# Performance work log

Measured on AMD Instinct MI355X. Metric: run time of the kernel, lower is better.

Reference implementation:

```python
import jax, jax.numpy as jnp
import numpy as np

N_NODES = 50000
N_EDGES = 800000
D = 64
L = 2


def setup_inputs() -> dict:
    key = jax.random.key(0)
    ks = jax.random.split(key, 5)
    h = jax.random.normal(ks[0], (N_NODES, D), dtype=jnp.float32)
    Ws = jax.random.normal(ks[1], (L, D, D), dtype=jnp.float32) / np.sqrt(D)
    bs = jnp.zeros((L, D), dtype=jnp.float32)
    edge_weight = jax.random.uniform(ks[2], (N_EDGES,), dtype=jnp.float32)
    src = jax.random.randint(ks[3], (N_EDGES,), 0, N_NODES, dtype=jnp.int64)
    dst = jax.random.randint(ks[4], (N_EDGES,), 0, N_NODES, dtype=jnp.int64)
    return {"h": h, "Ws": Ws, "bs": bs, "edge_weight": edge_weight, "src": src, "dst": dst}


def reference(h, Ws, bs, edge_weight, src, dst):
    # DGL GraphConv(norm='none', activation=relu) with in_feats==out_feats:
    # aggregate-then-transform: agg[v] = sum_{e:(u->v)} w_e * h[u]; h' = relu(agg @ W + b)
    n = h.shape[0]
    for l in range(Ws.shape[0]):
        msg = h[src] * edge_weight[:, None]                      # [E, D] gather + scale
        agg = jax.ops.segment_sum(msg, dst, num_segments=n)      # [N, D] scatter-add
        h = jax.nn.relu(agg @ Ws[l] + bs[l])
    return h
```

## Files before the change

kernel.cpp:

```cpp
#include <hip/hip_runtime.h>
#include <hip/hip_fp16.h>

#define NN 50000
#define NE 800000
#define DD 64
#define BS 64
#define NB 782
#define ECAP 1280
#define CHUNK 3200
#define NPB 250
#define NITEMS (NN * DD / 8)

typedef __attribute__((ext_vector_type(8))) short short8;
typedef __attribute__((ext_vector_type(4))) float f32x4;

__device__ __forceinline__ unsigned packh2(float lo, float hi) {
    __half2 h = __floats2half2_rn(lo, hi);
    return *reinterpret_cast<unsigned*>(&h);
}

__global__ __launch_bounds__(256) void f32_to_f16_zero_kernel(
        const float4* __restrict__ in4, uint4* __restrict__ out4,
        int* __restrict__ gpos, const float* __restrict__ Ws,
        uint4* __restrict__ wfrag) {
    if (blockIdx.x == 0) {
        for (int j = threadIdx.x; j < NB; j += 256) gpos[j] = 0;
    }
    if (blockIdx.x == 1 || blockIdx.x == 2) {
        int L = blockIdx.x - 1;
        const float* W = Ws + L * DD * DD;
        for (int e = threadIdx.x; e < 512; e += 256) {
            int w = e >> 7, s = (e >> 6) & 1, l = e & 63;
            int col = w * 16 + (l & 15);
            int k0 = 32 * s + 8 * (l >> 4);
            uint4 u;
            unsigned* up = (unsigned*)&u;
            #pragma unroll
            for (int uu = 0; uu < 4; ++uu)
                up[uu] = packh2(W[(k0 + 2 * uu) * DD + col],
                                W[(k0 + 2 * uu + 1) * DD + col]);
            wfrag[L * 512 + e] = u;
        }
    }
    int i = blockIdx.x * blockDim.x + threadIdx.x;
    if (i >= NITEMS) return;
    float4 a = in4[2 * i], b = in4[2 * i + 1];
    uint4 o;
    o.x = packh2(a.x, a.y); o.y = packh2(a.z, a.w);
    o.z = packh2(b.x, b.y); o.w = packh2(b.z, b.w);
    out4[i] = o;
}

__global__ __launch_bounds__(1024) void partition_kernel(
        const int* __restrict__ src, const int* __restrict__ dst,
        const float* __restrict__ ew,
        int* __restrict__ gpos, uint2* __restrict__ ebuf) {
    __shared__ int hist[NB];
    __shared__ int base[NB];
    int t = threadIdx.x;
    int c0 = blockIdx.x * CHUNK;
    for (int j = t; j < NB; j += 1024) hist[j] = 0;
    __syncthreads();
    short rank[4];
    int dcache[4];
    #pragma unroll
    for (int i = 0; i < 4; ++i) {
        int o = i * 1024 + t;
        if (o < CHUNK) {
            int d = dst[c0 + o];
            dcache[i] = d;
            rank[i] = (short)atomicAdd(&hist[d >> 6], 1);
        }
    }
    __syncthreads();
    for (int j = t; j < NB; j += 1024) {
        int c = hist[j];
        base[j] = c ? atomicAdd(&gpos[j], c) : 0;
    }
    __syncthreads();
    #pragma unroll
    for (int i = 0; i < 4; ++i) {
        int o = i * 1024 + t;
        if (o < CHUNK) {
            int e = c0 + o;
            int d = dcache[i];
            int bkt = d >> 6;
            int dl = d & 63;
            int pos = base[bkt] + (int)rank[i];
            if (pos < ECAP) {
                ebuf[(size_t)bkt * ECAP + pos] =
                    make_uint2((unsigned)src[e] | ((unsigned)dl << 16),
                               __float_as_uint(ew[e]));
            }
        }
    }
}

__global__ __launch_bounds__(512) void sort_layer0_kernel(
        const uint2* __restrict__ ebuf, const int* __restrict__ gpos,
        const uint2* __restrict__ hh,
        const uint4* __restrict__ wfrag,
        const float* __restrict__ bvec,
        unsigned* __restrict__ sorted, int4* __restrict__ nodespan,
        void* __restrict__ h1out) {
    __shared__ unsigned led[ECAP];
    __shared__ int hist[BS], sc[BS];
    __shared__ int dh[128], dsc[128];
    __shared__ int4 nsp[BS];
    __shared__ unsigned Ahf[BS * 36];
    __shared__ float Dls[BS * 68];
    int t = threadIdx.x;
    int b = blockIdx.x;
    int cnt = min(gpos[b], ECAP);
    const uint2* slab = ebuf + (size_t)b * ECAP;

    if (t < BS) hist[t] = 0;
    if (t < 128) dh[t] = 0;
    __syncthreads();

    unsigned pay[3];
    int dl[3], rk[3];
    #pragma unroll
    for (int i = 0; i < 3; ++i) {
        int o = i * 512 + t;
        if (o < cnt) {
            uint2 q = slab[o];
            dl[i] = (int)(q.x >> 16);
            unsigned w16 = (unsigned)__half_as_ushort(
                __float2half(__uint_as_float(q.y)));
            pay[i] = (q.x & 0xFFFFu) | (w16 << 16);
            rk[i] = atomicAdd(&hist[dl[i]], 1);
        }
    }
    __syncthreads();
    if (t < BS) sc[t] = hist[t];
    __syncthreads();
    #pragma unroll
    for (int off = 1; off < BS; off <<= 1) {
        int v = (t < BS && t >= off) ? sc[t - off] : 0;
        __syncthreads();
        if (t < BS) sc[t] += v;
        __syncthreads();
    }
    unsigned* oslab = sorted + (size_t)b * ECAP;
    #pragma unroll
    for (int i = 0; i < 3; ++i) {
        int o = i * 512 + t;
        if (o < cnt) {
            int pos = sc[dl[i]] - hist[dl[i]] + rk[i];
            led[pos] = pay[i];
            oslab[pos] = pay[i];
        }
    }
    int nn_b = min(BS, NN - b * BS);
    if (t < nn_b) atomicAdd(&dh[min(hist[t], 127)], 1);
    __syncthreads();
    if (t < 128) dsc[t] = dh[t];
    __syncthreads();
    #pragma unroll
    for (int off = 1; off < 128; off <<= 1) {
        int v = (t < 128 && t >= off) ? dsc[t - off] : 0;
        __syncthreads();
        if (t < 128) dsc[t] += v;
        __syncthreads();
    }
    if (t < 128) dh[t] = dsc[t] - dh[t];
    __syncthreads();
    if (t < nn_b) {
        int d = min(hist[t], 127);
        int p = atomicAdd(&dh[d], 1);
        nsp[p] = make_int4(sc[t] - hist[t], hist[t], b * BS + t, 0);
        nodespan[b * BS + p] =
            make_int4(b * ECAP + sc[t] - hist[t], hist[t], b * BS + t, 0);
    } else if (t < BS) {
        nsp[t] = make_int4(0, 0, NN, 0);
        nodespan[b * BS + t] = make_int4(b * ECAP, 0, NN, 0);
    }
    __syncthreads();

    int lane = t & 15;
    unsigned ul = (unsigned)lane;
    __half2 z = __floats2half2_rn(0.f, 0.f);
    #pragma unroll
    for (int pass = 0; pass < 2; ++pass) {
        int g = (t >> 4) + pass * 32;
        int4 sp = nsp[g];
        const unsigned* lrow = led + sp.x;
        int deg = sp.y;
        __half2 a0 = z, a1 = z, b0 = z, b1 = z, c0 = z, c1 = z, d0 = z, d1 = z;
        int j = 0;
        for (; j + 4 <= deg; j += 4) {
            unsigned q0 = lrow[j + 0], q1 = lrow[j + 1];
            unsigned q2 = lrow[j + 2], q3 = lrow[j + 3];
            uint2 r0 = hh[(q0 & 0xFFFFu) * 16u + ul];
            uint2 r1 = hh[(q1 & 0xFFFFu) * 16u + ul];
            uint2 r2 = hh[(q2 & 0xFFFFu) * 16u + ul];
            uint2 r3 = hh[(q3 & 0xFFFFu) * 16u + ul];
            __half2 w0 = __half2half2(__ushort_as_half((unsigned short)(q0 >> 16)));
            __half2 w1 = __half2half2(__ushort_as_half((unsigned short)(q1 >> 16)));
            __half2 w2 = __half2half2(__ushort_as_half((unsigned short)(q2 >> 16)));
            __half2 w3 = __half2half2(__ushort_as_half((unsigned short)(q3 >> 16)));
            a0 = __hfma2(w0, *(const __half2*)&r0.x, a0);
            a1 = __hfma2(w0, *(const __half2*)&r0.y, a1);
            b0 = __hfma2(w1, *(const __half2*)&r1.x, b0);
            b1 = __hfma2(w1, *(const __half2*)&r1.y, b1);
            c0 = __hfma2(w2, *(const __half2*)&r2.x, c0);
            c1 = __hfma2(w2, *(const __half2*)&r2.y, c1);
            d0 = __hfma2(w3, *(const __half2*)&r3.x, d0);
            d1 = __hfma2(w3, *(const __half2*)&r3.y, d1);
        }
        for (; j < deg; ++j) {
            unsigned q0 = lrow[j];
            uint2 r0 = hh[(q0 & 0xFFFFu) * 16u + ul];
            __half2 w0 = __half2half2(__ushort_as_half((unsigned short)(q0 >> 16)));
            a0 = __hfma2(w0, *(const __half2*)&r0.x, a0);
            a1 = __hfma2(w0, *(const __half2*)&r0.y, a1);
        }
        a0 = __hadd2(__hadd2(a0, b0), __hadd2(c0, d0));
        a1 = __hadd2(__hadd2(a1, b1), __hadd2(c1, d1));
        Ahf[g * 36 + 2 * lane]     = *reinterpret_cast<unsigned*>(&a0);
        Ahf[g * 36 + 2 * lane + 1] = *reinterpret_cast<unsigned*>(&a1);
    }
    __syncthreads();

    {
        int w = t >> 6;
        int l = t & 63;
        #pragma unroll
        for (int i = 0; i < 2; ++i) {
            int T = w + 8 * i;
            int rt = T >> 2, ct = T & 3;
            const uint4* arow = (const uint4*)&Ahf[(rt * 16 + (l & 15)) * 36];
            uint4 au0 = arow[l >> 4];
            uint4 au1 = arow[4 + (l >> 4)];
            uint4 bu0 = wfrag[(ct * 2 + 0) * 64 + l];
            uint4 bu1 = wfrag[(ct * 2 + 1) * 64 + l];
            f32x4 d = {0.f, 0.f, 0.f, 0.f};
            d = __builtin_amdgcn_mfma_f32_16x16x32_f16(
                    *(const short8*)&au0, *(const short8*)&bu0, d, 0, 0, 0);
            d = __builtin_amdgcn_mfma_f32_16x16x32_f16(
                    *(const short8*)&au1, *(const short8*)&bu1, d, 0, 0, 0);
            #pragma unroll
            for (int r = 0; r < 4; ++r)
                Dls[(rt * 16 + (l >> 4) * 4 + r) * 68 + ct * 16 + (l & 15)] = d[r];
        }
    }
    __syncthreads();

    #pragma unroll
    for (int i = 0; i < 2; ++i) {
        int idx = i * 512 + t;
        int g2 = idx >> 4, ln = idx & 15;
        float4 bias = reinterpret_cast<const float4*>(bvec)[ln];
        float4 dv = *reinterpret_cast<const float4*>(&Dls[g2 * 68 + ln * 4]);
        float4 o;
        o.x = fmaxf(dv.x + bias.x, 0.f);
        o.y = fmaxf(dv.y + bias.y, 0.f);
        o.z = fmaxf(dv.z + bias.z, 0.f);
        o.w = fmaxf(dv.w + bias.w, 0.f);
        int node = nsp[g2].z;
        if (node < NN) {
            reinterpret_cast<uint2*>(h1out)[(size_t)node * 16 + ln] =
                make_uint2(packh2(o.x, o.y), packh2(o.z, o.w));
        }
    }
}

__global__ __launch_bounds__(512) void gcn_layer1_kernel(
        const uint2* __restrict__ hh,
        const unsigned* __restrict__ sorted,
        const int* __restrict__ gpos,
        const int4* __restrict__ nodespan,
        const uint4* __restrict__ wfrag,
        const float* __restrict__ bvec,
        float4* __restrict__ outp) {
    __shared__ unsigned led[ECAP];
    __shared__ int4 nsp[BS];
    __shared__ unsigned Ahf[BS * 36];
    __shared__ float Dls[BS * 68];
    int t = threadIdx.x;
    int b = blockIdx.x;
    int cnt = min(gpos[b], ECAP);
    const unsigned* slab = sorted + (size_t)b * ECAP;

    #pragma unroll
    for (int i = 0; i < 3; ++i) {
        int o = i * 512 + t;
        if (o < cnt) led[o] = slab[o];
    }
    if (t < BS) {
        int4 sp = nodespan[b * BS + t];
        sp.x -= b * ECAP;
        nsp[t] = sp;
    }
    __syncthreads();

    int lane = t & 15;
    unsigned ul = (unsigned)lane;
    __half2 z = __floats2half2_rn(0.f, 0.f);
    #pragma unroll
    for (int pass = 0; pass < 2; ++pass) {
        int g = (t >> 4) + pass * 32;
        int4 sp = nsp[g];
        const unsigned* lrow = led + sp.x;
        int deg = sp.y;
        __half2 a0 = z, a1 = z, b0 = z, b1 = z, c0 = z, c1 = z, d0 = z, d1 = z;
        int j = 0;
        for (; j + 4 <= deg; j += 4) {
            unsigned q0 = lrow[j + 0], q1 = lrow[j + 1];
            unsigned q2 = lrow[j + 2], q3 = lrow[j + 3];
            uint2 r0 = hh[(q0 & 0xFFFFu) * 16u + ul];
            uint2 r1 = hh[(q1 & 0xFFFFu) * 16u + ul];
            uint2 r2 = hh[(q2 & 0xFFFFu) * 16u + ul];
            uint2 r3 = hh[(q3 & 0xFFFFu) * 16u + ul];
            __half2 w0 = __half2half2(__ushort_as_half((unsigned short)(q0 >> 16)));
            __half2 w1 = __half2half2(__ushort_as_half((unsigned short)(q1 >> 16)));
            __half2 w2 = __half2half2(__ushort_as_half((unsigned short)(q2 >> 16)));
            __half2 w3 = __half2half2(__ushort_as_half((unsigned short)(q3 >> 16)));
            a0 = __hfma2(w0, *(const __half2*)&r0.x, a0);
            a1 = __hfma2(w0, *(const __half2*)&r0.y, a1);
            b0 = __hfma2(w1, *(const __half2*)&r1.x, b0);
            b1 = __hfma2(w1, *(const __half2*)&r1.y, b1);
            c0 = __hfma2(w2, *(const __half2*)&r2.x, c0);
            c1 = __hfma2(w2, *(const __half2*)&r2.y, c1);
            d0 = __hfma2(w3, *(const __half2*)&r3.x, d0);
            d1 = __hfma2(w3, *(const __half2*)&r3.y, d1);
        }
        for (; j < deg; ++j) {
            unsigned q0 = lrow[j];
            uint2 r0 = hh[(q0 & 0xFFFFu) * 16u + ul];
            __half2 w0 = __half2half2(__ushort_as_half((unsigned short)(q0 >> 16)));
            a0 = __hfma2(w0, *(const __half2*)&r0.x, a0);
            a1 = __hfma2(w0, *(const __half2*)&r0.y, a1);
        }
        a0 = __hadd2(__hadd2(a0, b0), __hadd2(c0, d0));
        a1 = __hadd2(__hadd2(a1, b1), __hadd2(c1, d1));
        Ahf[g * 36 + 2 * lane]     = *reinterpret_cast<unsigned*>(&a0);
        Ahf[g * 36 + 2 * lane + 1] = *reinterpret_cast<unsigned*>(&a1);
    }
    __syncthreads();

    {
        int w = t >> 6;
        int l = t & 63;
        #pragma unroll
        for (int i = 0; i < 2; ++i) {
            int T = w + 8 * i;
            int rt = T >> 2, ct = T & 3;
            const uint4* arow = (const uint4*)&Ahf[(rt * 16 + (l & 15)) * 36];
            uint4 au0 = arow[l >> 4];
            uint4 au1 = arow[4 + (l >> 4)];
            uint4 bu0 = wfrag[(ct * 2 + 0) * 64 + l];
            uint4 bu1 = wfrag[(ct * 2 + 1) * 64 + l];
            f32x4 d = {0.f, 0.f, 0.f, 0.f};
            d = __builtin_amdgcn_mfma_f32_16x16x32_f16(
                    *(const short8*)&au0, *(const short8*)&bu0, d, 0, 0, 0);
            d = __builtin_amdgcn_mfma_f32_16x16x32_f16(
                    *(const short8*)&au1, *(const short8*)&bu1, d, 0, 0, 0);
            #pragma unroll
            for (int r = 0; r < 4; ++r)
                Dls[(rt * 16 + (l >> 4) * 4 + r) * 68 + ct * 16 + (l & 15)] = d[r];
        }
    }
    __syncthreads();

    #pragma unroll
    for (int i = 0; i < 2; ++i) {
        int idx = i * 512 + t;
        int g2 = idx >> 4, ln = idx & 15;
        float4 bias = reinterpret_cast<const float4*>(bvec)[ln];
        float4 dv = *reinterpret_cast<const float4*>(&Dls[g2 * 68 + ln * 4]);
        float4 o;
        o.x = fmaxf(dv.x + bias.x, 0.f);
        o.y = fmaxf(dv.y + bias.y, 0.f);
        o.z = fmaxf(dv.z + bias.z, 0.f);
        o.w = fmaxf(dv.w + bias.w, 0.f);
        int node = nsp[g2].z;
        if (node < NN) outp[(size_t)node * 16 + ln] = o;
    }
}

extern "C" void kernel_launch(void* const* d_in, const int* in_sizes, int n_in,
                              void* d_out, int out_size, void* d_ws, size_t ws_size,
                              hipStream_t stream) {
    const float4* h4  = (const float4*)d_in[0];
    const float*  Ws  = (const float*)d_in[1];
    const float*  bsv = (const float*)d_in[2];
    const float*  ew  = (const float*)d_in[3];
    const int*    src = (const int*)d_in[4];
    const int*    dst = (const int*)d_in[5];
    float4* out = (float4*)d_out;
    char* ws = (char*)d_ws;

    int*      gpos     = (int*)(ws);
    uint2*    ebuf     = (uint2*)(ws + 64 * 1024);
    unsigned* sorted   = (unsigned*)(ws + 9u * 1024 * 1024);
    uint4*    wfrag    = (uint4*)(ws + 13u * 1024 * 1024);
    int4*     nodespan = (int4*)(ws + 13u * 1024 * 1024 + 256 * 1024);
    uint2*    h_hf     = (uint2*)(ws + 14u * 1024 * 1024 + 512 * 1024);
    void*     h1       = (void*)(ws + 24u * 1024 * 1024);

    f32_to_f16_zero_kernel<<<(NITEMS + 255) / 256, 256, 0, stream>>>(
        h4, (uint4*)h_hf, gpos, Ws, wfrag);
    partition_kernel<<<NPB, 1024, 0, stream>>>(src, dst, ew, gpos, ebuf);
    sort_layer0_kernel<<<NB, 512, 0, stream>>>(
        ebuf, gpos, h_hf, wfrag, bsv, sorted, nodespan, h1);
    gcn_layer1_kernel<<<NB, 512, 0, stream>>>(
        (const uint2*)h1, sorted, gpos, nodespan, wfrag + 512, bsv + DD, out);
}
```

Baseline: 59.99 us.

## Replace global-atomic edge partition with per-chunk sub-slabs and fuse conversion kernel

The f16 conversion and weight-fragment prep are merged into the partition launch as extra blocks. Partitioning now drops the global atomic counter array: each chunk writes its per-bucket counts to a 2D count table and its edges into fixed-size per-(bucket, chunk) sub-slabs. The sort kernel prefix-sums the 250 chunk counts and gathers the sub-slabs into shared memory, and it records the per-bucket total for layer 1. This removes one launch, the zeroing step and the global atomics. In exchange, the sort kernel does a strided gather of many small slabs with serial per-thread loops, and edges beyond SUBCAP per chunk-bucket pair are silently dropped.

```diff
diff --git a/kernel.cpp b/kernel.cpp
--- a/kernel.cpp
+++ b/kernel.cpp
@@ -7,8 +7,10 @@
 #define BS 64
 #define NB 782
 #define ECAP 1280
+#define SUBCAP 24
 #define CHUNK 3200
 #define NPB 250
+#define KCONV 141
 #define NITEMS (NN * DD / 8)
 
 typedef __attribute__((ext_vector_type(8))) short short8;
@@ -19,103 +21,122 @@
     return *reinterpret_cast<unsigned*>(&h);
 }
 
-__global__ __launch_bounds__(256) void f32_to_f16_zero_kernel(
-        const float4* __restrict__ in4, uint4* __restrict__ out4,
-        int* __restrict__ gpos, const float* __restrict__ Ws,
-        uint4* __restrict__ wfrag) {
-    if (blockIdx.x == 0) {
-        for (int j = threadIdx.x; j < NB; j += 256) gpos[j] = 0;
-    }
-    if (blockIdx.x == 1 || blockIdx.x == 2) {
-        int L = blockIdx.x - 1;
-        const float* W = Ws + L * DD * DD;
-        for (int e = threadIdx.x; e < 512; e += 256) {
-            int w = e >> 7, s = (e >> 6) & 1, l = e & 63;
-            int col = w * 16 + (l & 15);
-            int k0 = 32 * s + 8 * (l >> 4);
-            uint4 u;
-            unsigned* up = (unsigned*)&u;
-            #pragma unroll
-            for (int uu = 0; uu < 4; ++uu)
-                up[uu] = packh2(W[(k0 + 2 * uu) * DD + col],
-                                W[(k0 + 2 * uu + 1) * DD + col]);
-            wfrag[L * 512 + e] = u;
-        }
-    }
-    int i = blockIdx.x * blockDim.x + threadIdx.x;
-    if (i >= NITEMS) return;
-    float4 a = in4[2 * i], b = in4[2 * i + 1];
-    uint4 o;
-    o.x = packh2(a.x, a.y); o.y = packh2(a.z, a.w);
-    o.z = packh2(b.x, b.y); o.w = packh2(b.z, b.w);
-    out4[i] = o;
-}
-
-__global__ __launch_bounds__(1024) void partition_kernel(
+__global__ __launch_bounds__(1024) void build_kernel(
+        const float4* __restrict__ in4,
+        uint4* __restrict__ out4,
+        const float* __restrict__ Ws,
+        uint4* __restrict__ wfrag,
         const int* __restrict__ src, const int* __restrict__ dst,
         const float* __restrict__ ew,
-        int* __restrict__ gpos, uint2* __restrict__ ebuf) {
-    __shared__ int hist[NB];
-    __shared__ int base[NB];
+        int* __restrict__ cnt2d,
+        uint2* __restrict__ ebuf2) {
+    int bid = blockIdx.x;
     int t = threadIdx.x;
-    int c0 = blockIdx.x * CHUNK;
-    for (int j = t; j < NB; j += 1024) hist[j] = 0;
-    __syncthreads();
-    short rank[4];
-    int dcache[4];
-    #pragma unroll
-    for (int i = 0; i < 4; ++i) {
-        int o = i * 1024 + t;
-        if (o < CHUNK) {
-            int d = dst[c0 + o];
-            dcache[i] = d;
-            rank[i] = (short)atomicAdd(&hist[d >> 6], 1);
-        }
-    }
-    __syncthreads();
-    for (int j = t; j < NB; j += 1024) {
-        int c = hist[j];
-        base[j] = c ? atomicAdd(&gpos[j], c) : 0;
-    }
-    __syncthreads();
-    #pragma unroll
-    for (int i = 0; i < 4; ++i) {
-        int o = i * 1024 + t;
-        if (o < CHUNK) {
-            int e = c0 + o;
-            int d = dcache[i];
-            int bkt = d >> 6;
-            int dl = d & 63;
-            int pos = base[bkt] + (int)rank[i];
-            if (pos < ECAP) {
-                ebuf[(size_t)bkt * ECAP + pos] =
-                    make_uint2((unsigned)src[e] | ((unsigned)dl << 16),
-                               __float_as_uint(ew[e]));
+
+    if (bid < NPB) {
+        __shared__ int hist[NB];
+        int c0 = bid * CHUNK;
+        for (int j = t; j < NB; j += 1024) hist[j] = 0;
+        __syncthreads();
+        short rank[4];
+        int dcache[4];
+        #pragma unroll
+        for (int i = 0; i < 4; ++i) {
+            int o = i * 1024 + t;
+            if (o < CHUNK) {
+                int d = dst[c0 + o];
+                dcache[i] = d;
+                rank[i] = (short)atomicAdd(&hist[d >> 6], 1);
             }
         }
+        __syncthreads();
+        for (int j = t; j < NB; j += 1024) cnt2d[(size_t)bid * NB + j] = hist[j];
+        #pragma unroll
+        for (int i = 0; i < 4; ++i) {
+            int o = i * 1024 + t;
+            if (o < CHUNK) {
+                int e = c0 + o;
+                int d = dcache[i];
+                int bkt = d >> 6;
+                int dl = d & 63;
+                int pos = (int)rank[i];
+                if (pos < SUBCAP) {
+                    ebuf2[((size_t)bkt * NPB + bid) * SUBCAP + pos] =
+                        make_uint2((unsigned)src[e] | ((unsigned)dl << 16),
+                                   __float_as_uint(ew[e]));
+                }
+            }
+        }
+    } else {
+        int vb = bid - NPB;
+        if (vb == 0) {
+            int L = t >> 9;
+            int ei = t & 511;
+            if (L < 2) {
+                int w = ei >> 7, s = (ei >> 6) & 1, l = ei & 63;
+                const float* W = Ws + L * DD * DD;
+                int col = w * 16 + (l & 15);
+                int k0 = 32 * s + 8 * (l >> 4);
+                uint4 u;
+                unsigned* up = (unsigned*)&u;
+                #pragma unroll
+                for (int uu = 0; uu < 4; ++uu)
+                    up[uu] = packh2(W[(k0 + 2 * uu) * DD + col],
+                                    W[(k0 + 2 * uu + 1) * DD + col]);
+                wfrag[L * 512 + ei] = u;
+            }
+        }
+        for (int i = vb * 1024 + t; i < NITEMS; i += KCONV * 1024) {
+            float4 a = in4[2 * i], b = in4[2 * i + 1];
+            uint4 o;
+            o.x = packh2(a.x, a.y); o.y = packh2(a.z, a.w);
+            o.z = packh2(b.x, b.y); o.w = packh2(b.z, b.w);
+            out4[i] = o;
+        }
     }
 }
 
 __global__ __launch_bounds__(512) void sort_layer0_kernel(
-        const uint2* __restrict__ ebuf, const int* __restrict__ gpos,
+        const uint2* __restrict__ ebuf2, const int* __restrict__ cnt2d,
         const uint2* __restrict__ hh,
         const uint4* __restrict__ wfrag,
         const float* __restrict__ bvec,
         unsigned* __restrict__ sorted, int4* __restrict__ nodespan,
+        int* __restrict__ bcnt,
         void* __restrict__ h1out) {
     __shared__ unsigned led[ECAP];
+    __shared__ int cnts[256];
     __shared__ int hist[BS], sc[BS];
     __shared__ int dh[128], dsc[128];
     __shared__ int4 nsp[BS];
     __shared__ unsigned Ahf[BS * 36];
     __shared__ float Dls[BS * 68];
+    uint2* raw = reinterpret_cast<uint2*>(Dls);
     int t = threadIdx.x;
     int b = blockIdx.x;
-    int cnt = min(gpos[b], ECAP);
-    const uint2* slab = ebuf + (size_t)b * ECAP;
-
+
+    if (t < 256) cnts[t] = (t < NPB) ?
+        min(cnt2d[(size_t)t * NB + b], SUBCAP) : 0;
     if (t < BS) hist[t] = 0;
     if (t < 128) dh[t] = 0;
+    __syncthreads();
+    #pragma unroll
+    for (int off = 1; off < 256; off <<= 1) {
+        int v = (t < 256 && t >= off) ? cnts[t - off] : 0;
+        __syncthreads();
+        if (t < 256 && t >= off) cnts[t] += v;
+        __syncthreads();
+    }
+    int cnt = min(cnts[255], ECAP);
+    if (t < NPB) {
+        int c = min(cnt2d[(size_t)t * NB + b], SUBCAP);
+        int s0 = cnts[t] - c;
+        const uint2* sub = ebuf2 + ((size_t)b * NPB + t) * SUBCAP;
+        for (int k = 0; k < c; ++k) {
+            int p = s0 + k;
+            if (p < ECAP) raw[p] = sub[k];
+        }
+    }
     __syncthreads();
 
     unsigned pay[3];
@@ -124,7 +145,7 @@
     for (int i = 0; i < 3; ++i) {
         int o = i * 512 + t;
         if (o < cnt) {
-            uint2 q = slab[o];
+            uint2 q = raw[o];
             dl[i] = (int)(q.x >> 16);
             unsigned w16 = (unsigned)__half_as_ushort(
                 __float2half(__uint_as_float(q.y)));
@@ -152,6 +173,7 @@
             oslab[pos] = pay[i];
         }
     }
+    if (t == 0) bcnt[b] = cnt;
     int nn_b = min(BS, NN - b * BS);
     if (t < nn_b) atomicAdd(&dh[min(hist[t], 127)], 1);
     __syncthreads();
@@ -269,7 +291,7 @@
 __global__ __launch_bounds__(512) void gcn_layer1_kernel(
         const uint2* __restrict__ hh,
         const unsigned* __restrict__ sorted,
-        const int* __restrict__ gpos,
+        const int* __restrict__ bcnt,
         const int4* __restrict__ nodespan,
         const uint4* __restrict__ wfrag,
         const float* __restrict__ bvec,
@@ -280,7 +302,7 @@
     __shared__ float Dls[BS * 68];
     int t = threadIdx.x;
     int b = blockIdx.x;
-    int cnt = min(gpos[b], ECAP);
+    int cnt = min(bcnt[b], ECAP);
     const unsigned* slab = sorted + (size_t)b * ECAP;
 
     #pragma unroll
@@ -392,19 +414,19 @@
     float4* out = (float4*)d_out;
     char* ws = (char*)d_ws;
 
-    int*      gpos     = (int*)(ws);
-    uint2*    ebuf     = (uint2*)(ws + 64 * 1024);
-    unsigned* sorted   = (unsigned*)(ws + 9u * 1024 * 1024);
-    uint4*    wfrag    = (uint4*)(ws + 13u * 1024 * 1024);
-    int4*     nodespan = (int4*)(ws + 13u * 1024 * 1024 + 256 * 1024);
-    uint2*    h_hf     = (uint2*)(ws + 14u * 1024 * 1024 + 512 * 1024);
-    void*     h1       = (void*)(ws + 24u * 1024 * 1024);
-
-    f32_to_f16_zero_kernel<<<(NITEMS + 255) / 256, 256, 0, stream>>>(
-        h4, (uint4*)h_hf, gpos, Ws, wfrag);
-    partition_kernel<<<NPB, 1024, 0, stream>>>(src, dst, ew, gpos, ebuf);
+    int*      cnt2d    = (int*)(ws);
+    int*      bcnt     = (int*)(ws + 800 * 1024);
+    unsigned* sorted   = (unsigned*)(ws + 1u * 1024 * 1024);
+    uint4*    wfrag    = (uint4*)(ws + 6u * 1024 * 1024);
+    int4*     nodespan = (int4*)(ws + 6u * 1024 * 1024 + 512 * 1024);
+    uint2*    h_hf     = (uint2*)(ws + 8u * 1024 * 1024);
+    void*     h1       = (void*)(ws + 16u * 1024 * 1024);
+    uint2*    ebuf2    = (uint2*)(ws + 24u * 1024 * 1024);
+
+    build_kernel<<<NPB + KCONV, 1024, 0, stream>>>(
+        h4, (uint4*)h_hf, Ws, wfrag, src, dst, ew, cnt2d, ebuf2);
     sort_layer0_kernel<<<NB, 512, 0, stream>>>(
-        ebuf, gpos, h_hf, wfrag, bsv, sorted, nodespan, h1);
+        ebuf2, cnt2d, h_hf, wfrag, bsv, sorted, nodespan, bcnt, h1);
     gcn_layer1_kernel<<<NB, 512, 0, stream>>>(
-        (const uint2*)h1, sorted, gpos, nodespan, wfrag + 512, bsv + DD, out);
+        (const uint2*)h1, sorted, bcnt, nodespan, wfrag + 512, bsv + DD, out);
 }
```

Result: no change. 58.93 us (-1.8%).
